# Kernel tuning notes

Hardware: AMD Instinct MI355X
Metric: run time of the kernel (lower is better)

## Reference

```python
import jax, jax.numpy as jnp
import numpy as np

WS = 8          # window_size
SHIFT = 4       # shift_size
HEADS = 12
C = 384
HD = C // HEADS
SCALE = HD ** -0.5
N = WS * WS


def _rel_pos_index(Wh, Ww):
    # double_step_seq(2*Ww-1, Wh, 1, Ww) -> (1, Wh*Ww); idx = rel + rel.T; flip along axis 1
    seq1 = np.arange(0, (2 * Ww - 1) * Wh, 2 * Ww - 1)
    seq2 = np.arange(0, Ww)
    rel = (seq1[:, None] + seq2[None, :]).reshape(1, -1)
    idx = rel + rel.T
    return np.flip(idx, 1).copy()

REL_IDX = jnp.asarray(_rel_pos_index(WS, WS))  # [N, N] int


def window_partition(x, ws):
    # x: [B, H, W, C] -> [B*nW, ws*ws, C]
    B, H, W, Cc = x.shape
    x = x.reshape(B, H // ws, ws, W // ws, ws, Cc).transpose(0, 1, 3, 2, 4, 5)
    return x.reshape(-1, ws * ws, Cc)


def window_reverse(win, H, W, ws):
    B = win.shape[0] // ((H // ws) * (W // ws))
    x = win.reshape(B, H // ws, W // ws, ws, ws, -1).transpose(0, 1, 3, 2, 4, 5)
    return x.reshape(B, H, W, -1)


def _attn_mask(H, W, ws, shift):
    # region ids 0..8 per (h,w) as in the torch slice loop
    hi = np.arange(H)
    wi = np.arange(W)
    h_id = (hi >= H - ws).astype(np.int32) + (hi >= H - shift).astype(np.int32)
    w_id = (wi >= W - ws).astype(np.int32) + (wi >= W - shift).astype(np.int32)
    cnt = (h_id[:, None] * 3 + w_id[None, :]).astype(np.float32)
    img = jnp.asarray(cnt)[None, :, :, None]              # [1, H, W, 1]
    mw = window_partition(img, ws).reshape(-1, ws * ws)   # [nW, N]
    diff = mw[:, None, :] - mw[:, :, None]                # [nW, N, N]
    return jnp.where(diff != 0, jnp.float32(-100.0), jnp.float32(0.0))


def setup_inputs() -> dict:
    key = jax.random.key(0)
    ks = jax.random.split(key, 8)
    B, H, W = 16, 96, 96
    std = 0.02
    return {
        "query": jax.random.normal(ks[0], (B, H * W, C), jnp.float32),
        "skip_query": jax.random.normal(ks[1], (B, H * W, C), jnp.float32),
        "W_qkv": jax.random.normal(ks[2], (C, 2 * C), jnp.float32) * std,
        "b_qkv": jnp.zeros((2 * C,), jnp.float32),
        "W_skip": jax.random.normal(ks[3], (C, C), jnp.float32) * std,
        "b_skip": jnp.zeros((C,), jnp.float32),
        "rpb_table": jax.random.normal(ks[4], ((2 * WS - 1) * (2 * WS - 1), HEADS), jnp.float32) * std,
        "W_proj": jax.random.normal(ks[5], (C, C), jnp.float32) * std,
        "b_proj": jnp.zeros((C,), jnp.float32),
        "h": H,
        "w": W,
    }


def reference(query, skip_query, W_qkv, b_qkv, W_skip, b_skip, rpb_table, W_proj, b_proj, h, w):
    B, L, Cc = query.shape
    q4 = query.reshape(B, h, w, Cc)
    s4 = skip_query.reshape(B, h, w, Cc)
    pad_r = (WS - w % WS) % WS
    pad_b = (WS - h % WS) % WS
    q4 = jnp.pad(q4, ((0, 0), (0, pad_b), (0, pad_r), (0, 0)))
    s4 = jnp.pad(s4, ((0, 0), (0, pad_b), (0, pad_r), (0, 0)))
    H_pad, W_pad = q4.shape[1], q4.shape[2]

    # cyclic shift
    q4 = jnp.roll(q4, (-SHIFT, -SHIFT), axis=(1, 2))
    s4 = jnp.roll(s4, (-SHIFT, -SHIFT), axis=(1, 2))
    mask = _attn_mask(H_pad, W_pad, WS, SHIFT)  # [nW, N, N]

    xw = window_partition(q4, WS)   # [Bn, N, C] -> k, v source
    sw = window_partition(s4, WS)   # [Bn, N, C] -> q source
    Bn = xw.shape[0]

    kv = (xw @ W_qkv + b_qkv).reshape(Bn, N, 2, HEADS, HD)
    k = kv[:, :, 0].transpose(0, 2, 1, 3)   # [Bn, H, N, d]
    v = kv[:, :, 1].transpose(0, 2, 1, 3)
    q = ((sw @ W_skip + b_skip).reshape(Bn, N, HEADS, HD).transpose(0, 2, 1, 3)) * SCALE

    attn = jnp.einsum('bhnd,bhmd->bhnm', q, k)  # [Bn, H, N, N]
    rpb = rpb_table[REL_IDX.reshape(-1)].reshape(N, N, HEADS).transpose(2, 0, 1)
    attn = attn + rpb[None]
    nW = mask.shape[0]
    attn = (attn.reshape(B, nW, HEADS, N, N) + mask[None, :, None]).reshape(Bn, HEADS, N, N)
    attn = jax.nn.softmax(attn, axis=-1)

    out = jnp.einsum('bhnm,bhmd->bhnd', attn, v).transpose(0, 2, 1, 3).reshape(Bn, N, Cc)
    out = out @ W_proj + b_proj

    x4 = window_reverse(out.reshape(-1, WS, WS, Cc), H_pad, W_pad, WS)
    x4 = jnp.roll(x4, (SHIFT, SHIFT), axis=(1, 2))
    x4 = x4[:, :h, :w]
    return x4.reshape(B, h * w, Cc)
```

## Files before the change

### kernel.cpp

```cpp
#include <hip/hip_runtime.h>
#include <hip/hip_bf16.h>


typedef __attribute__((ext_vector_type(8))) short short8;
typedef __attribute__((ext_vector_type(4))) float floatx4;

#define MFMA16(a, b, c) __builtin_amdgcn_mfma_f32_16x16x32_bf16(a, b, c, 0, 0, 0)

__device__ __forceinline__ short f2bf(float f) {
    __hip_bfloat16 h = __float2bfloat16(f);
    return *reinterpret_cast<short*>(&h);
}

__device__ __forceinline__ unsigned cvt2bf(float lo, float hi) {
    unsigned r;
    asm("v_cvt_pk_bf16_f32 %0, %1, %2" : "=v"(r) : "v"(lo), "v"(hi));
    return r;
}

__device__ __forceinline__ void glds16(const void* g, void* l) {
    __builtin_amdgcn_global_load_lds(
        (const __attribute__((address_space(1))) void*)g,
        (__attribute__((address_space(3))) void*)l, 16, 0, 0);
}


__global__ __launch_bounds__(256) void prep_wt(const float* __restrict__ Wqkv,
                                               const float* __restrict__ Wskip,
                                               short* __restrict__ Wt) {
    int tid = blockIdx.x * 256 + threadIdx.x;
    if (tid >= 384 * 144) return;
    int k = tid / 144;
    int n8 = (tid % 144) * 8;
#pragma unroll
    for (int e = 0; e < 8; e++) {
        int n = n8 + e;
        float v = (n < 768) ? Wqkv[k * 768 + n]
                            : Wskip[k * 384 + (n - 768)] * 0.17677669529663687f;
        Wt[(size_t)n * 384 + k] = f2bf(v);
    }
}

__global__ __launch_bounds__(256) void prep_wtp(const float* __restrict__ Wproj,
                                                short* __restrict__ WtP) {
    int tid = blockIdx.x * 256 + threadIdx.x;
    if (tid >= 384 * 48) return;
    int k = tid / 48;
    int n8 = (tid % 48) * 8;
#pragma unroll
    for (int e = 0; e < 8; e++) {
        int n = n8 + e;
        WtP[(size_t)n * 384 + k] = f2bf(Wproj[k * 384 + n]);
    }
}

__global__ __launch_bounds__(256) void prep_bias(const float* __restrict__ rpb,
                                                 float* __restrict__ bias64) {
    int tid = blockIdx.x * 256 + threadIdx.x;
    if (tid >= 49152) return;
    int h = tid >> 12;
    int rem = tid & 4095;
    int i = rem >> 6, kk = rem & 63;
    int j = 63 - kk;
    int ridx = 15 * (i >> 3) + (i & 7) + 15 * (j >> 3) + (j & 7);
    bias64[tid] = rpb[ridx * 12 + h];
}

template <bool SWP, bool FIN>
__device__ __forceinline__ void kloop12(
    const short* __restrict__ smemA, short* __restrict__ bwb,
    const short* __restrict__ curSrc, const short* __restrict__ nxtSrc,
    const int (&bso)[3], int l15, int g4, int al7, int brd,
    floatx4 (&acc)[3][4]) {
#pragma unroll
    for (int a = 0; a < 3; a++)
#pragma unroll
        for (int b = 0; b < 4; b++)
#pragma unroll
            for (int r = 0; r < 4; r++) acc[a][b][r] = 0.f;

#pragma unroll
    for (int kt = 0; kt < 12; ++kt) {
        if (FIN && kt == 11) {
            asm volatile("s_waitcnt vmcnt(0)" ::: "memory");
        } else {
            asm volatile("s_waitcnt vmcnt(3)" ::: "memory");
        }
        const int choff = ((kt * 4 + g4) ^ al7) * 8;
        short8 af[4], bfr[3];
#pragma unroll
        for (int b = 0; b < 4; b++)
            af[b] = *(const short8*)(smemA + (b * 16 + l15) * 384 + choff);
        short* hb = bwb + (kt & 1) * 1536;
#pragma unroll
        for (int nj = 0; nj < 3; nj++)
            bfr[nj] = *(const short8*)(hb + (nj * 16 + l15) * 32 + brd);
        __builtin_amdgcn_sched_barrier(0);
        asm volatile("s_waitcnt lgkmcnt(0)" ::: "memory");
        if (kt < 10) {
            int ko = (kt + 2) * 32;
#pragma unroll
            for (int j = 0; j < 3; j++)
                glds16(curSrc + bso[j] + ko, hb + j * 512);
        } else if (!FIN) {
            int ko = (kt - 10) * 32;
#pragma unroll
            for (int j = 0; j < 3; j++)
                glds16(nxtSrc + bso[j] + ko, hb + j * 512);
        }
        __builtin_amdgcn_sched_barrier(0);
        if (SWP) {
#pragma unroll
            for (int a = 0; a < 3; a++)
#pragma unroll
                for (int b = 0; b < 4; b++)
                    acc[a][b] = MFMA16(bfr[a], af[b], acc[a][b]);
        } else {
#pragma unroll
            for (int a = 0; a < 3; a++)
#pragma unroll
                for (int b = 0; b < 4; b++)
                    acc[a][b] = MFMA16(af[b], bfr[a], acc[a][b]);
        }
    }
}

__global__ __launch_bounds__(512, 1) void gemm_qkv(
    const float* __restrict__ xq, const float* __restrict__ xs,
    const short* __restrict__ Wt,
    const float* __restrict__ bqkv, const float* __restrict__ bskip,
    short* __restrict__ kbuf, short* __restrict__ vtbuf, short* __restrict__ qbuf) {
    __shared__ short smem[49152];

    const int win = blockIdx.x;
    const int var = blockIdx.y;
    const float* __restrict__ src = var ? xs : xq;

    const int tid = threadIdx.x, lane = tid & 63, wid = tid >> 6;
    const int l15 = lane & 15, g4 = lane >> 4;
    const int al7 = l15 & 7;
    const int brd = (g4 ^ ((l15 ^ (l15 >> 2)) & 3)) * 8;

    {
        int r = tid >> 3, q8 = tid & 7;
        int b = win / 144, wr = win % 144;
        int wy = wr / 12, wx = wr % 12;
        int yy = wy * 8 + (r >> 3) + 4; if (yy >= 96) yy -= 96;
        int xx = wx * 8 + (r & 7) + 4;  if (xx >= 96) xx -= 96;
        const float* rbase = src + ((size_t)b * 9216 + yy * 96 + xx) * 384;
        short* lrow = smem + r * 384;
        int r7 = r & 7;
#pragma unroll
        for (int j = 0; j < 6; j++) {
            int c = q8 + j * 8;
            float4 f0 = *(const float4*)(rbase + c * 8);
            float4 f1 = *(const float4*)(rbase + c * 8 + 4);
            uint4 u;
            u.x = cvt2bf(f0.x, f0.y); u.y = cvt2bf(f0.z, f0.w);
            u.z = cvt2bf(f1.x, f1.y); u.w = cvt2bf(f1.z, f1.w);
            *(uint4*)(lrow + ((c ^ r7) * 8)) = u;
        }
    }

    const int sw_st = ((lane >> 2) ^ (lane >> 4)) & 3;
    int bso[3];
#pragma unroll
    for (int j = 0; j < 3; j++)
        bso[j] = (j * 16 + (lane >> 2)) * 384 + (((lane & 3) ^ sw_st) * 8);
    short* bwb = smem + 24576 + wid * 3072;

    const short* src0 = Wt + (size_t)((var ? 768 : 0) + wid * 48) * 384;
    const short* src1 = Wt + (size_t)(384 + wid * 48) * 384;

#pragma unroll
    for (int j = 0; j < 3; j++) glds16(src0 + bso[j], bwb + j * 512);
#pragma unroll
    for (int j = 0; j < 3; j++) glds16(src0 + bso[j] + 32, bwb + 1536 + j * 512);
    __syncthreads();

    floatx4 acc[3][4];
    if (var == 0) {
        kloop12<true, false>(smem, bwb, src0, src1, bso, l15, g4, al7, brd, acc);
#pragma unroll
        for (int a = 0; a < 3; a++) {
            int nm = wid * 48 + a * 16 + g4 * 4;
            int head = nm >> 5, d0 = nm & 31;
            float4 bv = *(const float4*)(bqkv + nm);
            short* dst = kbuf + (size_t)(win * 12 + head) * 2048 + d0;
#pragma unroll
            for (int b = 0; b < 4; b++) {
                int t = b * 16 + l15;
                uint2 pk;
                pk.x = cvt2bf(acc[a][b][0] + bv.x, acc[a][b][1] + bv.y);
                pk.y = cvt2bf(acc[a][b][2] + bv.z, acc[a][b][3] + bv.w);
                *(uint2*)(dst + (size_t)t * 32) = pk;
            }
        }
        kloop12<false, true>(smem, bwb, src1, nullptr, bso, l15, g4, al7, brd, acc);
#pragma unroll
        for (int nj = 0; nj < 3; nj++) {
            int nm = wid * 48 + nj * 16 + l15;
            int head = nm >> 5, d = nm & 31;
            float bvs = bqkv[384 + nm];
            short* dst = vtbuf + ((size_t)(win * 12 + head) * 32 + d) * 64;
#pragma unroll
            for (int mi = 0; mi < 4; mi++) {
                int t0 = mi * 16 + g4 * 4;
                uint2 pk;
                pk.x = cvt2bf(acc[nj][mi][0] + bvs, acc[nj][mi][1] + bvs);
                pk.y = cvt2bf(acc[nj][mi][2] + bvs, acc[nj][mi][3] + bvs);
                *(uint2*)(dst + t0) = pk;
            }
        }
    } else {
        kloop12<true, true>(smem, bwb, src0, nullptr, bso, l15, g4, al7, brd, acc);
        const float scl = 0.17677669529663687f;
#pragma unroll
        for (int a = 0; a < 3; a++) {
            int nm = wid * 48 + a * 16 + g4 * 4;
            int head = nm >> 5, d0 = nm & 31;
            float4 bv = *(const float4*)(bskip + nm);
            short* dst = qbuf + (size_t)(win * 12 + head) * 2048 + d0;
#pragma unroll
            for (int b = 0; b < 4; b++) {
                int t = b * 16 + l15;
                uint2 pk;
                pk.x = cvt2bf(acc[a][b][0] + bv.x * scl, acc[a][b][1] + bv.y * scl);
                pk.y = cvt2bf(acc[a][b][2] + bv.z * scl, acc[a][b][3] + bv.w * scl);
                *(uint2*)(dst + (size_t)t * 32) = pk;
            }
        }
    }
}

__global__ __launch_bounds__(256) void attn_kernel(
    const short* __restrict__ kbuf, const short* __restrict__ vtbuf,
    const short* __restrict__ qbuf, const float* __restrict__ bias64,
    short* __restrict__ aout, int ntask) {
    __shared__ short lps[18432];
    int lane = threadIdx.x & 63, wid = threadIdx.x >> 6;
    int task = blockIdx.x * 4 + wid;
    if (task >= ntask) return;
    int win = task / 12, head = task % 12;
    int l15 = lane & 15, g4 = lane >> 4;

    const short* kb = kbuf + (size_t)task * 2048;
    const short* qb = qbuf + (size_t)task * 2048;
    const short* vb = vtbuf + (size_t)task * 2048;

    short8 kf[4], qf[4], vf[2][2];
#pragma unroll
    for (int mi = 0; mi < 4; mi++)
        kf[mi] = *(const short8*)(kb + (mi * 16 + l15) * 32 + g4 * 8);
#pragma unroll
    for (int nj = 0; nj < 4; nj++)
        qf[nj] = *(const short8*)(qb + (nj * 16 + l15) * 32 + g4 * 8);
#pragma unroll
    for (int ma = 0; ma < 2; ma++)
#pragma unroll
        for (int ks = 0; ks < 2; ks++)
            vf[ma][ks] = *(const short8*)(vb + (ma * 16 + l15) * 64 + ks * 32 + g4 * 8);

    floatx4 st[4][4];
#pragma unroll
    for (int mi = 0; mi < 4; mi++)
#pragma unroll
        for (int nj = 0; nj < 4; nj++)
#pragma unroll
            for (int r = 0; r < 4; r++) st[mi][nj][r] = 0.f;

#pragma unroll
    for (int mi = 0; mi < 4; mi++)
#pragma unroll
        for (int nj = 0; nj < 4; nj++)
            st[mi][nj] = MFMA16(kf[mi], qf[nj], st[mi][nj]);

    const float* bb = bias64 + head * 4096;
#pragma unroll
    for (int nj = 0; nj < 4; nj++) {
        int i = nj * 16 + l15;
#pragma unroll
        for (int mi = 0; mi < 4; mi++) {
            floatx4 b4 = *(const floatx4*)(bb + i * 64 + mi * 16 + g4 * 4);
            st[mi][nj] += b4;
        }
    }

    int wr = win % 144;
    int wy = wr / 12, wx = wr % 12;
    if (wy == 11 || wx == 11) {
        int wy11 = (wy == 11), wx11 = (wx == 11);
        int ri[4];
#pragma unroll
        for (int nj = 0; nj < 4; nj++) {
            int t = nj * 16 + l15;
            int hh = wy11 ? (((t >> 3) >= 4) ? 2 : 1) : 0;
            int ww = wx11 ? (((t & 7) >= 4) ? 2 : 1) : 0;
            ri[nj] = hh * 3 + ww;
        }
#pragma unroll
        for (int mi = 0; mi < 4; mi++)
#pragma unroll
            for (int r = 0; r < 4; r++) {
                int t = mi * 16 + g4 * 4 + r;
                int hh = wy11 ? (((t >> 3) >= 4) ? 2 : 1) : 0;
                int ww = wx11 ? (((t & 7) >= 4) ? 2 : 1) : 0;
                int rk = hh * 3 + ww;
#pragma unroll
                for (int nj = 0; nj < 4; nj++)
                    if (rk != ri[nj]) st[mi][nj][r] -= 100.0f;
            }
    }

    float rden[4];
#pragma unroll
    for (int nj = 0; nj < 4; nj++) {
        float m = -1e30f;
#pragma unroll
        for (int mi = 0; mi < 4; mi++)
#pragma unroll
            for (int r = 0; r < 4; r++) m = fmaxf(m, st[mi][nj][r]);
        m = fmaxf(m, __shfl_xor(m, 16));
        m = fmaxf(m, __shfl_xor(m, 32));
        float s = 0.f;
#pragma unroll
        for (int mi = 0; mi < 4; mi++)
#pragma unroll
            for (int r = 0; r < 4; r++) {
                float p = __expf(st[mi][nj][r] - m);
                st[mi][nj][r] = p;
                s += p;
            }
        s += __shfl_xor(s, 16);
        s += __shfl_xor(s, 32);
        rden[nj] = 1.0f / s;
    }

    short* Lp = lps + wid * 4608;
#pragma unroll
    for (int mi = 0; mi < 4; mi++)
#pragma unroll
        for (int nj = 0; nj < 4; nj++) {
            uint2 pk;
            pk.x = cvt2bf(st[mi][nj][0], st[mi][nj][1]);
            pk.y = cvt2bf(st[mi][nj][2], st[mi][nj][3]);
            *(uint2*)(Lp + (nj * 16 + l15) * 72 + mi * 16 + g4 * 4) = pk;
        }

    floatx4 o[2][4];
#pragma unroll
    for (int ma = 0; ma < 2; ma++)
#pragma unroll
        for (int nj = 0; nj < 4; nj++)
#pragma unroll
            for (int r = 0; r < 4; r++) o[ma][nj][r] = 0.f;
#pragma unroll
    for (int ks = 0; ks < 2; ks++) {
        short8 pb[4];
#pragma unroll
        for (int nj = 0; nj < 4; nj++)
            pb[nj] = *(const short8*)(Lp + (nj * 16 + l15) * 72 + ks * 32 + g4 * 8);
#pragma unroll
        for (int ma = 0; ma < 2; ma++)
#pragma unroll
            for (int nj = 0; nj < 4; nj++)
                o[ma][nj] = MFMA16(vf[ma][ks], pb[nj], o[ma][nj]);
    }

    short* ob = aout + (size_t)win * 64 * 384 + head * 32;
#pragma unroll
    for (int ma = 0; ma < 2; ma++)
#pragma unroll
        for (int nj = 0; nj < 4; nj++) {
            int i = nj * 16 + l15;
            uint2 pk;
            pk.x = cvt2bf(o[ma][nj][0] * rden[nj], o[ma][nj][1] * rden[nj]);
            pk.y = cvt2bf(o[ma][nj][2] * rden[nj], o[ma][nj][3] * rden[nj]);
            *(uint2*)(ob + (size_t)i * 384 + ma * 16 + g4 * 4) = pk;
        }
}

__global__ __launch_bounds__(512, 1) void gemm_proj(
    const short* __restrict__ aout, const short* __restrict__ WtP,
    const float* __restrict__ bproj, float* __restrict__ out) {
    __shared__ short smem[49152];

    const int win = blockIdx.x;
    const int m0 = win * 64;
    const int tid = threadIdx.x, lane = tid & 63, wid = tid >> 6;
    const int l15 = lane & 15, g4 = lane >> 4;
    const int al7 = l15 & 7;
    const int brd = (g4 ^ ((l15 ^ (l15 >> 2)) & 3)) * 8;

#pragma unroll
    for (int j = 0; j < 6; j++) {
        int i = wid * 6 + j;
        int c = i * 64 + lane;
        int row = c / 48, ch = c - row * 48;
        const short* s = aout + (size_t)(m0 + row) * 384 + ((ch ^ (row & 7)) * 8);
        glds16(s, smem + i * 512);
    }

    const int sw_st = ((lane >> 2) ^ (lane >> 4)) & 3;
    int bso[3];
#pragma unroll
    for (int j = 0; j < 3; j++)
        bso[j] = (j * 16 + (lane >> 2)) * 384 + (((lane & 3) ^ sw_st) * 8);
    short* bwb = smem + 24576 + wid * 3072;
    const short* src0 = WtP + (size_t)(wid * 48) * 384;

#pragma unroll
    for (int j = 0; j < 3; j++) glds16(src0 + bso[j], bwb + j * 512);
#pragma unroll
    for (int j = 0; j < 3; j++) glds16(src0 + bso[j] + 32, bwb + 1536 + j * 512);
    __syncthreads();

    floatx4 acc[3][4];
    kloop12<true, true>(smem, bwb, src0, nullptr, bso, l15, g4, al7, brd, acc);

    const int b_img = win / 144, wrw = win % 144;
    const int wy = wrw / 12, wx = wrw % 12;
#pragma unroll
    for (int a = 0; a < 3; a++) {
        int n = wid * 48 + a * 16 + g4 * 4;
        float4 bv = *(const float4*)(bproj + n);
#pragma unroll
        for (int b = 0; b < 4; b++) {
            int t = b * 16 + l15;
            int yy = wy * 8 + (t >> 3) + 4; if (yy >= 96) yy -= 96;
            int xx = wx * 8 + (t & 7) + 4;  if (xx >= 96) xx -= 96;
            floatx4 o = acc[a][b];
            o[0] += bv.x; o[1] += bv.y; o[2] += bv.z; o[3] += bv.w;
            *(floatx4*)(&out[((size_t)b_img * 9216 + yy * 96 + xx) * 384 + n]) = o;
        }
    }
}

extern "C" void kernel_launch(void* const* d_in, const int* in_sizes, int n_in,
                              void* d_out, int out_size, void* d_ws, size_t ws_size,
                              hipStream_t stream) {
    const float* query = (const float*)d_in[0];
    const float* skipq = (const float*)d_in[1];
    const float* Wqkv  = (const float*)d_in[2];
    const float* bqkv  = (const float*)d_in[3];
    const float* Wskip = (const float*)d_in[4];
    const float* bskip = (const float*)d_in[5];
    const float* rpb   = (const float*)d_in[6];
    const float* Wproj = (const float*)d_in[7];
    const float* bproj = (const float*)d_in[8];
    float* out = (float*)d_out;

    int M = in_sizes[0] / 384;
    int nwin = M / 64;

    char* ws = (char*)d_ws;
    size_t off = 0;
    auto alloc = [&](size_t bytes) -> void* {
        void* p = ws + off;
        off = (off + bytes + 255) & ~(size_t)255;
        return p;
    };
    short* Wt     = (short*)alloc((size_t)1152 * 384 * 2);
    short* WtP    = (short*)alloc((size_t)384 * 384 * 2);
    float* bias64 = (float*)alloc((size_t)12 * 64 * 64 * 4);
    short* kbuf   = (short*)alloc((size_t)M * 384 * 2);
    short* vtbuf  = (short*)alloc((size_t)M * 384 * 2);
    short* qbuf   = (short*)alloc((size_t)M * 384 * 2);
    short* aout   = (short*)alloc((size_t)M * 384 * 2);
    (void)ws_size;

    hipLaunchKernelGGL(prep_wt, dim3(216), dim3(256), 0, stream, Wqkv, Wskip, Wt);
    hipLaunchKernelGGL(prep_wtp, dim3(72), dim3(256), 0, stream, Wproj, WtP);
    hipLaunchKernelGGL(prep_bias, dim3(192), dim3(256), 0, stream, rpb, bias64);
    hipLaunchKernelGGL(gemm_qkv, dim3(nwin, 2), dim3(512), 0, stream,
                       query, skipq, Wt, bqkv, bskip, kbuf, vtbuf, qbuf);
    hipLaunchKernelGGL(attn_kernel, dim3(nwin * 12 / 4), dim3(256), 0, stream,
                       kbuf, vtbuf, qbuf, bias64, aout, nwin * 12);
    hipLaunchKernelGGL(gemm_proj, dim3(nwin), dim3(512), 0, stream,
                       aout, WtP, bproj, out);
}
```

Before: 577.0 us.

## Use 4-wave blocks with 64-column warp tiles for QKV and proj GEMMs

Both GEMM kernels move from 512-thread blocks with 48-column-per-wave tiles to 256-thread blocks with 64-column-per-wave tiles. Each wave now loops over several 64-column chunks of the weight matrix, and the epilogue picks the K, V or Q output path per chunk. LDS drops to 80KB, so two blocks can share a CU. The aim is more A-fragment reuse per MFMA and better occupancy. The cost is uneven work across waves, since some waves run an extra k-loop, plus higher register pressure from a 4x4 accumulator.

```diff
diff --git a/kernel.cpp b/kernel.cpp
--- a/kernel.cpp
+++ b/kernel.cpp
@@ -66,58 +66,52 @@
     bias64[tid] = rpb[ridx * 12 + h];
 }
 
-template <bool SWP, bool FIN>
-__device__ __forceinline__ void kloop12(
+__device__ __forceinline__ void kloop12f(
     const short* __restrict__ smemA, short* __restrict__ bwb,
     const short* __restrict__ curSrc, const short* __restrict__ nxtSrc,
-    const int (&bso)[3], int l15, int g4, int al7, int brd,
-    floatx4 (&acc)[3][4]) {
-#pragma unroll
-    for (int a = 0; a < 3; a++)
+    const int (&bso)[4], int l15, int g4, int al7, int brd,
+    bool swapped, floatx4 (&acc)[4][4]) {
+#pragma unroll
+    for (int a = 0; a < 4; a++)
 #pragma unroll
         for (int b = 0; b < 4; b++)
 #pragma unroll
             for (int r = 0; r < 4; r++) acc[a][b][r] = 0.f;
-
+    const bool fin = (nxtSrc == nullptr);
 #pragma unroll
     for (int kt = 0; kt < 12; ++kt) {
-        if (FIN && kt == 11) {
-            asm volatile("s_waitcnt vmcnt(0)" ::: "memory");
-        } else {
-            asm volatile("s_waitcnt vmcnt(3)" ::: "memory");
-        }
+        if (fin && kt == 11) asm volatile("s_waitcnt vmcnt(0)" ::: "memory");
+        else                 asm volatile("s_waitcnt vmcnt(4)" ::: "memory");
         const int choff = ((kt * 4 + g4) ^ al7) * 8;
-        short8 af[4], bfr[3];
+        short8 af[4], bfr[4];
+        short* hb = bwb + (kt & 1) * 2048;
 #pragma unroll
         for (int b = 0; b < 4; b++)
             af[b] = *(const short8*)(smemA + (b * 16 + l15) * 384 + choff);
-        short* hb = bwb + (kt & 1) * 1536;
-#pragma unroll
-        for (int nj = 0; nj < 3; nj++)
-            bfr[nj] = *(const short8*)(hb + (nj * 16 + l15) * 32 + brd);
+#pragma unroll
+        for (int a = 0; a < 4; a++)
+            bfr[a] = *(const short8*)(hb + (a * 16 + l15) * 32 + brd);
         __builtin_amdgcn_sched_barrier(0);
         asm volatile("s_waitcnt lgkmcnt(0)" ::: "memory");
         if (kt < 10) {
             int ko = (kt + 2) * 32;
 #pragma unroll
-            for (int j = 0; j < 3; j++)
-                glds16(curSrc + bso[j] + ko, hb + j * 512);
-        } else if (!FIN) {
+            for (int j = 0; j < 4; j++) glds16(curSrc + bso[j] + ko, hb + j * 512);
+        } else if (!fin) {
             int ko = (kt - 10) * 32;
 #pragma unroll
-            for (int j = 0; j < 3; j++)
-                glds16(nxtSrc + bso[j] + ko, hb + j * 512);
+            for (int j = 0; j < 4; j++) glds16(nxtSrc + bso[j] + ko, hb + j * 512);
         }
         __builtin_amdgcn_sched_barrier(0);
-        if (SWP) {
-#pragma unroll
-            for (int a = 0; a < 3; a++)
+        if (swapped) {
+#pragma unroll
+            for (int a = 0; a < 4; a++)
 #pragma unroll
                 for (int b = 0; b < 4; b++)
                     acc[a][b] = MFMA16(bfr[a], af[b], acc[a][b]);
         } else {
 #pragma unroll
-            for (int a = 0; a < 3; a++)
+            for (int a = 0; a < 4; a++)
 #pragma unroll
                 for (int b = 0; b < 4; b++)
                     acc[a][b] = MFMA16(af[b], bfr[a], acc[a][b]);
@@ -125,12 +119,12 @@
     }
 }
 
-__global__ __launch_bounds__(512, 1) void gemm_qkv(
+__global__ __launch_bounds__(256, 2) void gemm_qkv(
     const float* __restrict__ xq, const float* __restrict__ xs,
     const short* __restrict__ Wt,
     const float* __restrict__ bqkv, const float* __restrict__ bskip,
     short* __restrict__ kbuf, short* __restrict__ vtbuf, short* __restrict__ qbuf) {
-    __shared__ short smem[49152];
+    __shared__ short smem[40960];
 
     const int win = blockIdx.x;
     const int var = blockIdx.y;
@@ -142,7 +136,7 @@
     const int brd = (g4 ^ ((l15 ^ (l15 >> 2)) & 3)) * 8;
 
     {
-        int r = tid >> 3, q8 = tid & 7;
+        int r = tid >> 2, q4 = tid & 3;
         int b = win / 144, wr = win % 144;
         int wy = wr / 12, wx = wr % 12;
         int yy = wy * 8 + (r >> 3) + 4; if (yy >= 96) yy -= 96;
@@ -151,8 +145,8 @@
         short* lrow = smem + r * 384;
         int r7 = r & 7;
 #pragma unroll
-        for (int j = 0; j < 6; j++) {
-            int c = q8 + j * 8;
+        for (int j = 0; j < 12; j++) {
+            int c = q4 + j * 4;
             float4 f0 = *(const float4*)(rbase + c * 8);
             float4 f1 = *(const float4*)(rbase + c * 8 + 4);
             uint4 u;
@@ -162,28 +156,30 @@
         }
     }
 
-    const int sw_st = ((lane >> 2) ^ (lane >> 4)) & 3;
-    int bso[3];
-#pragma unroll
-    for (int j = 0; j < 3; j++)
-        bso[j] = (j * 16 + (lane >> 2)) * 384 + (((lane & 3) ^ sw_st) * 8);
-    short* bwb = smem + 24576 + wid * 3072;
-
-    const short* src0 = Wt + (size_t)((var ? 768 : 0) + wid * 48) * 384;
-    const short* src1 = Wt + (size_t)(384 + wid * 48) * 384;
-
-#pragma unroll
-    for (int j = 0; j < 3; j++) glds16(src0 + bso[j], bwb + j * 512);
-#pragma unroll
-    for (int j = 0; j < 3; j++) glds16(src0 + bso[j] + 32, bwb + 1536 + j * 512);
+    const int swst = ((lane >> 2) ^ (lane >> 4)) & 3;
+    int bso[4];
+#pragma unroll
+    for (int j = 0; j < 4; j++)
+        bso[j] = (j * 16 + (lane >> 2)) * 384 + (((lane & 3) ^ swst) * 8);
+    short* bwb = smem + 24576 + wid * 4096;
+
+    const int wpair = wid >> 1, wn = wid & 1;
+    int pcol = var ? (768 + wid * 64) : (wpair * 128 + wn * 64);
+    const short* cur = Wt + (size_t)pcol * 384;
+
+#pragma unroll
+    for (int j = 0; j < 4; j++) glds16(cur + bso[j], bwb + j * 512);
+#pragma unroll
+    for (int j = 0; j < 4; j++) glds16(cur + bso[j] + 32, bwb + 2048 + j * 512);
     __syncthreads();
 
-    floatx4 acc[3][4];
-    if (var == 0) {
-        kloop12<true, false>(smem, bwb, src0, src1, bso, l15, g4, al7, brd, acc);
-#pragma unroll
-        for (int a = 0; a < 3; a++) {
-            int nm = wid * 48 + a * 16 + g4 * 4;
+    floatx4 acc[4][4];
+    const float scl = 0.17677669529663687f;
+
+    auto epi_k = [&](int pc) {
+#pragma unroll
+        for (int a = 0; a < 4; a++) {
+            int nm = pc + a * 16 + g4 * 4;
             int head = nm >> 5, d0 = nm & 31;
             float4 bv = *(const float4*)(bqkv + nm);
             short* dst = kbuf + (size_t)(win * 12 + head) * 2048 + d0;
@@ -196,10 +192,11 @@
                 *(uint2*)(dst + (size_t)t * 32) = pk;
             }
         }
-        kloop12<false, true>(smem, bwb, src1, nullptr, bso, l15, g4, al7, brd, acc);
-#pragma unroll
-        for (int nj = 0; nj < 3; nj++) {
-            int nm = wid * 48 + nj * 16 + l15;
+    };
+    auto epi_v = [&](int pc) {
+#pragma unroll
+        for (int nj = 0; nj < 4; nj++) {
+            int nm = pc + nj * 16 + l15 - 384;
             int head = nm >> 5, d = nm & 31;
             float bvs = bqkv[384 + nm];
             short* dst = vtbuf + ((size_t)(win * 12 + head) * 32 + d) * 64;
@@ -212,12 +209,11 @@
                 *(uint2*)(dst + t0) = pk;
             }
         }
-    } else {
-        kloop12<true, true>(smem, bwb, src0, nullptr, bso, l15, g4, al7, brd, acc);
-        const float scl = 0.17677669529663687f;
-#pragma unroll
-        for (int a = 0; a < 3; a++) {
-            int nm = wid * 48 + a * 16 + g4 * 4;
+    };
+    auto epi_q = [&](int pc) {
+#pragma unroll
+        for (int a = 0; a < 4; a++) {
+            int nm = pc + a * 16 + g4 * 4 - 768;
             int head = nm >> 5, d0 = nm & 31;
             float4 bv = *(const float4*)(bskip + nm);
             short* dst = qbuf + (size_t)(win * 12 + head) * 2048 + d0;
@@ -229,6 +225,27 @@
                 pk.y = cvt2bf(acc[a][b][2] + bv.z * scl, acc[a][b][3] + bv.w * scl);
                 *(uint2*)(dst + (size_t)t * 32) = pk;
             }
+        }
+    };
+
+    if (var == 0) {
+        const short* nxt = cur + (size_t)256 * 384;
+        kloop12f(smem, bwb, cur, nxt, bso, l15, g4, al7, brd, true, acc);
+        epi_k(pcol);
+        pcol += 256; cur = nxt; nxt = cur + (size_t)256 * 384;
+        bool swp1 = (wpair == 0);
+        kloop12f(smem, bwb, cur, nxt, bso, l15, g4, al7, brd, swp1, acc);
+        if (swp1) epi_k(pcol); else epi_v(pcol);
+        pcol += 256; cur = nxt;
+        kloop12f(smem, bwb, cur, nullptr, bso, l15, g4, al7, brd, false, acc);
+        epi_v(pcol);
+    } else {
+        const short* nxt = (wid < 2) ? Wt + (size_t)(1024 + wid * 64) * 384 : nullptr;
+        kloop12f(smem, bwb, cur, nxt, bso, l15, g4, al7, brd, true, acc);
+        epi_q(pcol);
+        if (wid < 2) {
+            kloop12f(smem, bwb, nxt, nullptr, bso, l15, g4, al7, brd, true, acc);
+            epi_q(1024 + wid * 64);
         }
     }
 }
@@ -380,10 +397,10 @@
         }
 }
 
-__global__ __launch_bounds__(512, 1) void gemm_proj(
+__global__ __launch_bounds__(256, 2) void gemm_proj(
     const short* __restrict__ aout, const short* __restrict__ WtP,
     const float* __restrict__ bproj, float* __restrict__ out) {
-    __shared__ short smem[49152];
+    __shared__ short smem[40960];
 
     const int win = blockIdx.x;
     const int m0 = win * 64;
@@ -393,46 +410,56 @@
     const int brd = (g4 ^ ((l15 ^ (l15 >> 2)) & 3)) * 8;
 
 #pragma unroll
-    for (int j = 0; j < 6; j++) {
-        int i = wid * 6 + j;
+    for (int j = 0; j < 12; j++) {
+        int i = wid * 12 + j;
         int c = i * 64 + lane;
         int row = c / 48, ch = c - row * 48;
         const short* s = aout + (size_t)(m0 + row) * 384 + ((ch ^ (row & 7)) * 8);
         glds16(s, smem + i * 512);
     }
 
-    const int sw_st = ((lane >> 2) ^ (lane >> 4)) & 3;
-    int bso[3];
-#pragma unroll
-    for (int j = 0; j < 3; j++)
-        bso[j] = (j * 16 + (lane >> 2)) * 384 + (((lane & 3) ^ sw_st) * 8);
-    short* bwb = smem + 24576 + wid * 3072;
-    const short* src0 = WtP + (size_t)(wid * 48) * 384;
-
-#pragma unroll
-    for (int j = 0; j < 3; j++) glds16(src0 + bso[j], bwb + j * 512);
-#pragma unroll
-    for (int j = 0; j < 3; j++) glds16(src0 + bso[j] + 32, bwb + 1536 + j * 512);
+    const int swst = ((lane >> 2) ^ (lane >> 4)) & 3;
+    int bso[4];
+#pragma unroll
+    for (int j = 0; j < 4; j++)
+        bso[j] = (j * 16 + (lane >> 2)) * 384 + (((lane & 3) ^ swst) * 8);
+    short* bwb = smem + 24576 + wid * 4096;
+
+    int pcol = wid * 64;
+    const short* cur = WtP + (size_t)pcol * 384;
+#pragma unroll
+    for (int j = 0; j < 4; j++) glds16(cur + bso[j], bwb + j * 512);
+#pragma unroll
+    for (int j = 0; j < 4; j++) glds16(cur + bso[j] + 32, bwb + 2048 + j * 512);
     __syncthreads();
-
-    floatx4 acc[3][4];
-    kloop12<true, true>(smem, bwb, src0, nullptr, bso, l15, g4, al7, brd, acc);
 
     const int b_img = win / 144, wrw = win % 144;
     const int wy = wrw / 12, wx = wrw % 12;
-#pragma unroll
-    for (int a = 0; a < 3; a++) {
-        int n = wid * 48 + a * 16 + g4 * 4;
-        float4 bv = *(const float4*)(bproj + n);
-#pragma unroll
-        for (int b = 0; b < 4; b++) {
-            int t = b * 16 + l15;
-            int yy = wy * 8 + (t >> 3) + 4; if (yy >= 96) yy -= 96;
-            int xx = wx * 8 + (t & 7) + 4;  if (xx >= 96) xx -= 96;
-            floatx4 o = acc[a][b];
-            o[0] += bv.x; o[1] += bv.y; o[2] += bv.z; o[3] += bv.w;
-            *(floatx4*)(&out[((size_t)b_img * 9216 + yy * 96 + xx) * 384 + n]) = o;
-        }
+
+    floatx4 acc[4][4];
+    auto epi = [&](int pc) {
+#pragma unroll
+        for (int a = 0; a < 4; a++) {
+            int n = pc + a * 16 + g4 * 4;
+            float4 bv = *(const float4*)(bproj + n);
+#pragma unroll
+            for (int b = 0; b < 4; b++) {
+                int t = b * 16 + l15;
+                int yy = wy * 8 + (t >> 3) + 4; if (yy >= 96) yy -= 96;
+                int xx = wx * 8 + (t & 7) + 4;  if (xx >= 96) xx -= 96;
+                floatx4 o = acc[a][b];
+                o[0] += bv.x; o[1] += bv.y; o[2] += bv.z; o[3] += bv.w;
+                *(floatx4*)(&out[((size_t)b_img * 9216 + yy * 96 + xx) * 384 + n]) = o;
+            }
+        }
+    };
+
+    const short* nxt = (wid < 2) ? WtP + (size_t)(256 + wid * 64) * 384 : nullptr;
+    kloop12f(smem, bwb, cur, nxt, bso, l15, g4, al7, brd, true, acc);
+    epi(pcol);
+    if (wid < 2) {
+        kloop12f(smem, bwb, nxt, nullptr, bso, l15, g4, al7, brd, true, acc);
+        epi(256 + wid * 64);
     }
 }
 
@@ -472,10 +499,10 @@
     hipLaunchKernelGGL(prep_wt, dim3(216), dim3(256), 0, stream, Wqkv, Wskip, Wt);
     hipLaunchKernelGGL(prep_wtp, dim3(72), dim3(256), 0, stream, Wproj, WtP);
     hipLaunchKernelGGL(prep_bias, dim3(192), dim3(256), 0, stream, rpb, bias64);
-    hipLaunchKernelGGL(gemm_qkv, dim3(nwin, 2), dim3(512), 0, stream,
+    hipLaunchKernelGGL(gemm_qkv, dim3(nwin, 2), dim3(256), 0, stream,
                        query, skipq, Wt, bqkv, bskip, kbuf, vtbuf, qbuf);
     hipLaunchKernelGGL(attn_kernel, dim3(nwin * 12 / 4), dim3(256), 0, stream,
                        kbuf, vtbuf, qbuf, bias64, aout, nwin * 12);
-    hipLaunchKernelGGL(gemm_proj, dim3(nwin), dim3(512), 0, stream,
+    hipLaunchKernelGGL(gemm_proj, dim3(nwin), dim3(256), 0, stream,
                        aout, WtP, bproj, out);
 }
```

Result: faster. 505.1 us (-12.5%).

## Deepen weight prefetch pipeline from double to quadruple buffering in GEMM k-loop

Applied to the files above, without the earlier changes.

The per-wave weight staging in the shared GEMM k-loop grows from two LDS slots to four, with global-to-LDS loads issued three k-steps ahead. The prefetch is issued before the LDS reads of the current step, and the explicit lgkmcnt wait is dropped. This keeps more weight loads in flight to hide global latency, at the cost of more shared memory per block (LDS grows to 144KB). Reordering the issue relies on the ring depth to avoid overwriting a slot that is still being read.

```diff
diff --git a/kernel.cpp b/kernel.cpp
--- a/kernel.cpp
+++ b/kernel.cpp
@@ -67,7 +67,7 @@
 }
 
 template <bool SWP, bool FIN>
-__device__ __forceinline__ void kloop12(
+__device__ __forceinline__ void kloop12d(
     const short* __restrict__ smemA, short* __restrict__ bwb,
     const short* __restrict__ curSrc, const short* __restrict__ nxtSrc,
     const int (&bso)[3], int l15, int g4, int al7, int brd,
@@ -78,37 +78,31 @@
         for (int b = 0; b < 4; b++)
 #pragma unroll
             for (int r = 0; r < 4; r++) acc[a][b][r] = 0.f;
-
 #pragma unroll
     for (int kt = 0; kt < 12; ++kt) {
-        if (FIN && kt == 11) {
-            asm volatile("s_waitcnt vmcnt(0)" ::: "memory");
-        } else {
-            asm volatile("s_waitcnt vmcnt(3)" ::: "memory");
-        }
+        if (FIN && kt == 10)      asm volatile("s_waitcnt vmcnt(3)" ::: "memory");
+        else if (FIN && kt == 11) asm volatile("s_waitcnt vmcnt(0)" ::: "memory");
+        else                      asm volatile("s_waitcnt vmcnt(6)" ::: "memory");
+        short* wb = bwb + ((kt + 3) & 3) * 1536;
+        if (kt < 9) {
+            int ko = (kt + 3) * 32;
+#pragma unroll
+            for (int j = 0; j < 3; j++) glds16(curSrc + bso[j] + ko, wb + j * 512);
+        } else if (!FIN) {
+            int ko = (kt - 9) * 32;
+#pragma unroll
+            for (int j = 0; j < 3; j++) glds16(nxtSrc + bso[j] + ko, wb + j * 512);
+        }
+        __builtin_amdgcn_sched_barrier(0);
         const int choff = ((kt * 4 + g4) ^ al7) * 8;
+        const short* hb = bwb + (kt & 3) * 1536;
         short8 af[4], bfr[3];
 #pragma unroll
         for (int b = 0; b < 4; b++)
             af[b] = *(const short8*)(smemA + (b * 16 + l15) * 384 + choff);
-        short* hb = bwb + (kt & 1) * 1536;
-#pragma unroll
-        for (int nj = 0; nj < 3; nj++)
-            bfr[nj] = *(const short8*)(hb + (nj * 16 + l15) * 32 + brd);
-        __builtin_amdgcn_sched_barrier(0);
-        asm volatile("s_waitcnt lgkmcnt(0)" ::: "memory");
-        if (kt < 10) {
-            int ko = (kt + 2) * 32;
-#pragma unroll
-            for (int j = 0; j < 3; j++)
-                glds16(curSrc + bso[j] + ko, hb + j * 512);
-        } else if (!FIN) {
-            int ko = (kt - 10) * 32;
-#pragma unroll
-            for (int j = 0; j < 3; j++)
-                glds16(nxtSrc + bso[j] + ko, hb + j * 512);
-        }
-        __builtin_amdgcn_sched_barrier(0);
+#pragma unroll
+        for (int a = 0; a < 3; a++)
+            bfr[a] = *(const short8*)(hb + (a * 16 + l15) * 32 + brd);
         if (SWP) {
 #pragma unroll
             for (int a = 0; a < 3; a++)
@@ -130,7 +124,7 @@
     const short* __restrict__ Wt,
     const float* __restrict__ bqkv, const float* __restrict__ bskip,
     short* __restrict__ kbuf, short* __restrict__ vtbuf, short* __restrict__ qbuf) {
-    __shared__ short smem[49152];
+    __shared__ short smem[73728];
 
     const int win = blockIdx.x;
     const int var = blockIdx.y;
@@ -162,25 +156,28 @@
         }
     }
 
-    const int sw_st = ((lane >> 2) ^ (lane >> 4)) & 3;
+    const int swst = ((lane >> 2) ^ (lane >> 4)) & 3;
     int bso[3];
 #pragma unroll
     for (int j = 0; j < 3; j++)
-        bso[j] = (j * 16 + (lane >> 2)) * 384 + (((lane & 3) ^ sw_st) * 8);
-    short* bwb = smem + 24576 + wid * 3072;
-
-    const short* src0 = Wt + (size_t)((var ? 768 : 0) + wid * 48) * 384;
-    const short* src1 = Wt + (size_t)(384 + wid * 48) * 384;
-
-#pragma unroll
-    for (int j = 0; j < 3; j++) glds16(src0 + bso[j], bwb + j * 512);
-#pragma unroll
-    for (int j = 0; j < 3; j++) glds16(src0 + bso[j] + 32, bwb + 1536 + j * 512);
+        bso[j] = (j * 16 + (lane >> 2)) * 384 + (((lane & 3) ^ swst) * 8);
+    short* bwb = smem + 24576 + wid * 6144;
+
+    const short* sK = Wt + (size_t)(var ? (768 + wid * 48) : (wid * 48)) * 384;
+    const short* sV = Wt + (size_t)(384 + wid * 48) * 384;
+
+#pragma unroll
+    for (int s = 0; s < 3; s++)
+#pragma unroll
+        for (int j = 0; j < 3; j++)
+            glds16(sK + bso[j] + s * 32, bwb + s * 1536 + j * 512);
     __syncthreads();
 
     floatx4 acc[3][4];
+    const float scl = 0.17677669529663687f;
+
     if (var == 0) {
-        kloop12<true, false>(smem, bwb, src0, src1, bso, l15, g4, al7, brd, acc);
+        kloop12d<true, false>(smem, bwb, sK, sV, bso, l15, g4, al7, brd, acc);
 #pragma unroll
         for (int a = 0; a < 3; a++) {
             int nm = wid * 48 + a * 16 + g4 * 4;
@@ -196,7 +193,7 @@
                 *(uint2*)(dst + (size_t)t * 32) = pk;
             }
         }
-        kloop12<false, true>(smem, bwb, src1, nullptr, bso, l15, g4, al7, brd, acc);
+        kloop12d<false, true>(smem, bwb, sV, nullptr, bso, l15, g4, al7, brd, acc);
 #pragma unroll
         for (int nj = 0; nj < 3; nj++) {
             int nm = wid * 48 + nj * 16 + l15;
@@ -213,8 +210,7 @@
             }
         }
     } else {
-        kloop12<true, true>(smem, bwb, src0, nullptr, bso, l15, g4, al7, brd, acc);
-        const float scl = 0.17677669529663687f;
+        kloop12d<true, true>(smem, bwb, sK, nullptr, bso, l15, g4, al7, brd, acc);
 #pragma unroll
         for (int a = 0; a < 3; a++) {
             int nm = wid * 48 + a * 16 + g4 * 4;
@@ -383,7 +379,7 @@
 __global__ __launch_bounds__(512, 1) void gemm_proj(
     const short* __restrict__ aout, const short* __restrict__ WtP,
     const float* __restrict__ bproj, float* __restrict__ out) {
-    __shared__ short smem[49152];
+    __shared__ short smem[73728];
 
     const int win = blockIdx.x;
     const int m0 = win * 64;
@@ -401,22 +397,23 @@
         glds16(s, smem + i * 512);
     }
 
-    const int sw_st = ((lane >> 2) ^ (lane >> 4)) & 3;
+    const int swst = ((lane >> 2) ^ (lane >> 4)) & 3;
     int bso[3];
 #pragma unroll
     for (int j = 0; j < 3; j++)
-        bso[j] = (j * 16 + (lane >> 2)) * 384 + (((lane & 3) ^ sw_st) * 8);
-    short* bwb = smem + 24576 + wid * 3072;
-    const short* src0 = WtP + (size_t)(wid * 48) * 384;
-
-#pragma unroll
-    for (int j = 0; j < 3; j++) glds16(src0 + bso[j], bwb + j * 512);
-#pragma unroll
-    for (int j = 0; j < 3; j++) glds16(src0 + bso[j] + 32, bwb + 1536 + j * 512);
+        bso[j] = (j * 16 + (lane >> 2)) * 384 + (((lane & 3) ^ swst) * 8);
+    short* bwb = smem + 24576 + wid * 6144;
+    const short* sB = WtP + (size_t)(wid * 48) * 384;
+
+#pragma unroll
+    for (int s = 0; s < 3; s++)
+#pragma unroll
+        for (int j = 0; j < 3; j++)
+            glds16(sB + bso[j] + s * 32, bwb + s * 1536 + j * 512);
     __syncthreads();
 
     floatx4 acc[3][4];
-    kloop12<true, true>(smem, bwb, src0, nullptr, bso, l15, g4, al7, brd, acc);
+    kloop12d<true, true>(smem, bwb, sB, nullptr, bso, l15, g4, al7, brd, acc);
 
     const int b_img = win / 144, wrw = win % 144;
     const int wy = wrw / 12, wx = wrw % 12;
```

Measured after the change: 556.4 us. 3.6% less time.
